# Kernel optimization log

Measured on AMD Instinct MI355X. Metric: run time of the kernel, lower is better.

The kernel has to match this reference:

```python
import jax, jax.numpy as jnp
import numpy as np


def setup_inputs() -> dict:
    key = jax.random.key(0)
    ks = jax.random.split(key, 8)
    N, E = 10000, 160000
    IN, OUT, TC = 512, 512, 256
    x = jax.random.normal(ks[0], (N, IN), dtype=jnp.float32)
    t_emb = jax.random.normal(ks[1], (TC,), dtype=jnp.float32)
    edge_index = jax.random.randint(ks[2], (2, E), 0, N, dtype=jnp.int64)
    # GCNConv weight (glorot-ish scale) and bias
    W = jax.random.normal(ks[3], (IN, OUT), dtype=jnp.float32) / np.sqrt(IN)
    b = jnp.zeros((OUT,), dtype=jnp.float32)
    # time_proj Linear(TC, OUT)
    Wt = jax.random.normal(ks[4], (TC, OUT), dtype=jnp.float32) / np.sqrt(TC)
    bt = jnp.zeros((OUT,), dtype=jnp.float32)
    return {"x": x, "t_emb": t_emb, "edge_index": edge_index,
            "W": W, "b": b, "Wt": Wt, "bt": bt}


def _gcn_conv(x, edge_index, W, b):
    # PyG GCNConv: add self-loops, symmetric normalization, xW, scatter-add, +bias
    N = x.shape[0]
    loops = jnp.arange(N, dtype=edge_index.dtype)
    src = jnp.concatenate([edge_index[0], loops])  # [E+N]
    dst = jnp.concatenate([edge_index[1], loops])
    deg = jax.ops.segment_sum(jnp.ones_like(dst, dtype=x.dtype), dst,
                              num_segments=N)  # in-degree incl. self-loop
    dinv = jnp.where(deg > 0, jax.lax.rsqrt(deg), 0.0)
    norm = dinv[src] * dinv[dst]  # [E+N]
    xw = x @ W  # [N, OUT] - transform before gather (fewer FLOPs on edges)
    msgs = norm[:, None] * xw[src]  # [E+N, OUT]
    out = jax.ops.segment_sum(msgs, dst, num_segments=N)
    return out + b


def reference(x, t_emb, edge_index, W, b, Wt, bt):
    h = _gcn_conv(x, edge_index, W, b)          # [N, OUT]
    time_emb = t_emb @ Wt + bt                   # [OUT] (1-D t_emb branch)
    return h + time_emb
```

## Files before the change

kernel.cpp:

```cpp
#include <hip/hip_runtime.h>

#define OUTC 512
#define INC 512
#define NTILE 4
#define TCOL 128
#define LDA 72
#define TPB 256
#define CAP 96

typedef __bf16 bf16x8 __attribute__((ext_vector_type(8)));
typedef float f32x4 __attribute__((ext_vector_type(4)));

static __device__ __forceinline__ unsigned short f2bf(float f) {
    unsigned u = __float_as_uint(f);
    unsigned r = u + 0x7fffu + ((u >> 16) & 1u);
    return (unsigned short)(r >> 16);
}
static __device__ __forceinline__ float bflo(unsigned r) { return __uint_as_float(r << 16); }
static __device__ __forceinline__ float bfhi(unsigned r) { return __uint_as_float(r & 0xffff0000u); }
static __device__ __forceinline__ void acc8s(float* a, uint4 v, float n) {
    a[0] += n * bflo(v.x); a[1] += n * bfhi(v.x);
    a[2] += n * bflo(v.y); a[3] += n * bfhi(v.y);
    a[4] += n * bflo(v.z); a[5] += n * bfhi(v.z);
    a[6] += n * bflo(v.w); a[7] += n * bfhi(v.w);
}

__global__ __launch_bounds__(256) void k_prep(const float* __restrict__ x,
                                              const float* __restrict__ W,
                                              const float* __restrict__ t_emb,
                                              const float* __restrict__ Wt,
                                              const float* __restrict__ bt,
                                              const float* __restrict__ b,
                                              int* __restrict__ counts,
                                              unsigned short* __restrict__ xb,
                                              unsigned short* __restrict__ wtb,
                                              float* __restrict__ temb,
                                              int ZB, int XBB,
                                              int M, int Mpad, int TC) {
    __shared__ float smem[32 * 33];
    int bid = blockIdx.x;
    if (bid < ZB) {
        int i = bid * 256 + threadIdx.x;
        if (i < M) counts[i] = 0;
    } else if (bid < ZB + XBB) {
        int idx = (bid - ZB) * 256 + threadIdx.x;
        int row = idx >> 6;
        int kg = (idx & 63) * 8;
        ushort4 h0 = make_ushort4(0, 0, 0, 0), h1 = make_ushort4(0, 0, 0, 0);
        if (row < M) {
            float4 v0 = *(const float4*)(x + (size_t)row * INC + kg);
            float4 v1 = *(const float4*)(x + (size_t)row * INC + kg + 4);
            h0 = make_ushort4(f2bf(v0.x), f2bf(v0.y), f2bf(v0.z), f2bf(v0.w));
            h1 = make_ushort4(f2bf(v1.x), f2bf(v1.y), f2bf(v1.z), f2bf(v1.w));
        }
        *(ushort4*)(xb + (size_t)row * INC + kg) = h0;
        *(ushort4*)(xb + (size_t)row * INC + kg + 4) = h1;
    } else if (bid < ZB + XBB + 256) {
        int b2 = bid - (ZB + XBB);
        int bk = (b2 & 15) * 32, bn = (b2 >> 4) * 32;
        int tx = threadIdx.x & 31, ty = threadIdx.x >> 5;
        for (int r = ty; r < 32; r += 8)
            smem[r * 33 + tx] = W[(size_t)(bk + r) * OUTC + bn + tx];
        __syncthreads();
        for (int r = ty; r < 32; r += 8)
            wtb[(size_t)(bn + r) * INC + bk + tx] = f2bf(smem[tx * 33 + r]);
    } else {
        int j = bid - (ZB + XBB + 256);
        int t = threadIdx.x;
        float p = 0.0f;
        for (int k = t; k < TC; k += 256) p += t_emb[k] * Wt[(size_t)k * OUTC + j];
        smem[t] = p;
        __syncthreads();
        for (int s = 128; s > 0; s >>= 1) {
            if (t < s) smem[t] += smem[t + s];
            __syncthreads();
        }
        if (t == 0) temb[j] = smem[0] + bt[j] + b[j];
    }
}

__global__ __launch_bounds__(256) void k_ag(const unsigned short* __restrict__ xb,
                                            const unsigned short* __restrict__ wtb,
                                            unsigned short* __restrict__ xwb,
                                            const int* __restrict__ src,
                                            const int* __restrict__ dst,
                                            int* __restrict__ counts,
                                            int* __restrict__ slots,
                                            int E, int Mpad) {
    __shared__ unsigned short la[128 * LDA];
    __shared__ unsigned short lb[64 * LDA];

    const int bid = blockIdx.x;
    const int tid = threadIdx.x;
    const int GB = (Mpad / 128) * 8;

    if (bid >= GB) {
        int e = (bid - GB) * 256 + tid;
        if (e < E) {
            int s = src[e];
            int d = dst[e];
            int pos = atomicAdd(&counts[d], 1);
            if (pos < CAP) slots[(size_t)d * CAP + pos] = s;
        }
        return;
    }

    const int n0 = (bid & 7) * 64;
    const int m0 = (bid >> 3) * 128;
    const int lane = tid & 63;
    const int wave = tid >> 6;
    const int wm = wave * 32;
    const int l15 = lane & 15;
    const int k8 = (lane >> 4) * 8;

    f32x4 acc[2][4];
#pragma unroll
    for (int t = 0; t < 2; ++t)
#pragma unroll
        for (int u = 0; u < 4; ++u)
            acc[t][u] = (f32x4){0.f, 0.f, 0.f, 0.f};

    for (int k0 = 0; k0 < INC; k0 += 64) {
#pragma unroll
        for (int i = 0; i < 4; ++i) {
            int f = i * 256 + tid;
            int row = f >> 3, c = f & 7;
            uint4 v = *(const uint4*)(xb + (size_t)(m0 + row) * INC + k0 + c * 8);
            *(uint4*)(&la[row * LDA + c * 8]) = v;
        }
#pragma unroll
        for (int i = 0; i < 2; ++i) {
            int f = i * 256 + tid;
            int row = f >> 3, c = f & 7;
            uint4 v = *(const uint4*)(wtb + (size_t)(n0 + row) * INC + k0 + c * 8);
            *(uint4*)(&lb[row * LDA + c * 8]) = v;
        }
        __syncthreads();

#pragma unroll
        for (int kc = 0; kc < 64; kc += 32) {
            bf16x8 af0 = *(const bf16x8*)(&la[(wm + l15) * LDA + kc + k8]);
            bf16x8 af1 = *(const bf16x8*)(&la[(wm + 16 + l15) * LDA + kc + k8]);
#pragma unroll
            for (int u = 0; u < 4; ++u) {
                bf16x8 bfr = *(const bf16x8*)(&lb[(u * 16 + l15) * LDA + kc + k8]);
                acc[0][u] = __builtin_amdgcn_mfma_f32_16x16x32_bf16(af0, bfr, acc[0][u], 0, 0, 0);
                acc[1][u] = __builtin_amdgcn_mfma_f32_16x16x32_bf16(af1, bfr, acc[1][u], 0, 0, 0);
            }
        }
        __syncthreads();
    }

    const int rbase = (lane >> 4) * 4;
#pragma unroll
    for (int t = 0; t < 2; ++t)
#pragma unroll
        for (int u = 0; u < 4; ++u) {
            int gcol = n0 + u * 16 + l15;
            unsigned short* p = xwb + (size_t)(gcol >> 7) * Mpad * TCOL + (gcol & 127);
#pragma unroll
            for (int r = 0; r < 4; ++r) {
                int grow = m0 + wm + t * 16 + rbase + r;
                p[(size_t)grow * TCOL] = f2bf(acc[t][u][r]);
            }
        }
}

__global__ __launch_bounds__(256) void k_gather(const int* __restrict__ slots,
                                                const int* __restrict__ counts,
                                                const unsigned short* __restrict__ xwb,
                                                const float* __restrict__ temb,
                                                float* __restrict__ out, int N, int Mpad) {
    const int bid = blockIdx.x;
    const int tile = (bid & 7) >> 1;
    const int node = (bid >> 3) * 8 + (bid & 1) * 4 + (threadIdx.x >> 6);
    if (node >= N) return;
    const int lane = threadIdx.x & 63;
    const int slot = lane >> 4;
    const int c8 = (lane & 15) * 8;
    const unsigned short* basep = xwb + (size_t)tile * Mpad * TCOL + c8;

    float a[8] = {0.f, 0.f, 0.f, 0.f, 0.f, 0.f, 0.f, 0.f};
    const int deg = counts[node];
    const int dc = deg < CAP ? deg : CAP;
    const int* sp = slots + (size_t)node * CAP;
    int i = 0;
    for (; i + 8 <= dc; i += 8) {
        int sA = sp[i + slot];
        int sB = sp[i + 4 + slot];
        uint4 vA = *(const uint4*)(basep + (size_t)sA * TCOL);
        uint4 vB = *(const uint4*)(basep + (size_t)sB * TCOL);
        float nA = rsqrtf((float)counts[sA] + 1.0f);
        float nB = rsqrtf((float)counts[sB] + 1.0f);
        acc8s(a, vA, nA);
        acc8s(a, vB, nB);
    }
    for (; i < dc; i += 4) {
        int idx = i + slot;
        int sA = node;
        float nA = 0.f;
        if (idx < dc) {
            sA = sp[idx];
            nA = rsqrtf((float)counts[sA] + 1.0f);
        }
        uint4 v = *(const uint4*)(basep + (size_t)sA * TCOL);
        acc8s(a, v, nA);
    }
#pragma unroll
    for (int k = 0; k < 8; ++k) {
        a[k] += __shfl_xor(a[k], 16, 64);
        a[k] += __shfl_xor(a[k], 32, 64);
    }
    const float di = rsqrtf((float)deg + 1.0f);
    {
        uint4 v = *(const uint4*)(basep + (size_t)node * TCOL);
        acc8s(a, v, di);
    }
    if (slot < 2) {
        const int gc = tile * TCOL + c8 + slot * 4;
        float4 tv = *(const float4*)(temb + gc);
        float4 o;
        o.x = di * a[slot * 4 + 0] + tv.x;
        o.y = di * a[slot * 4 + 1] + tv.y;
        o.z = di * a[slot * 4 + 2] + tv.z;
        o.w = di * a[slot * 4 + 3] + tv.w;
        *(float4*)(out + (size_t)node * OUTC + gc) = o;
    }
}

extern "C" void kernel_launch(void* const* d_in, const int* in_sizes, int n_in,
                              void* d_out, int out_size, void* d_ws, size_t ws_size,
                              hipStream_t stream) {
    const float* x     = (const float*)d_in[0];
    const float* t_emb = (const float*)d_in[1];
    const int*   ei    = (const int*)d_in[2];
    const float* W     = (const float*)d_in[3];
    const float* b     = (const float*)d_in[4];
    const float* Wt    = (const float*)d_in[5];
    const float* bt    = (const float*)d_in[6];
    float* out = (float*)d_out;

    const int N  = in_sizes[0] / INC;
    const int E  = in_sizes[2] / 2;
    const int TC = in_sizes[1];
    const int Mpad = (N + 127) & ~127;

    char* ws = (char*)d_ws;
    size_t off = 0;
    unsigned short* xb  = (unsigned short*)(ws + off); off += (size_t)Mpad * INC * 2;
    unsigned short* xwb = (unsigned short*)(ws + off); off += (size_t)Mpad * OUTC * 2;
    unsigned short* wtb = (unsigned short*)(ws + off); off += (size_t)INC * OUTC * 2;
    int* counts = (int*)(ws + off);        off += ((size_t)N * 4 + 255) & ~(size_t)255;
    int* slots  = (int*)(ws + off);        off += ((size_t)N * CAP * 4 + 255) & ~(size_t)255;
    float* temb = (float*)(ws + off);      off += OUTC * 4;

    const int* srcIdx = ei;
    const int* dstIdx = ei + E;

    const int ZB  = (N + 255) / 256;
    const int XBB = Mpad * (INC / 8) / 256;
    const int GB  = (Mpad / 128) * 8;
    const int SB  = (E + 255) / 256;

    k_prep<<<ZB + XBB + 256 + OUTC, TPB, 0, stream>>>(x, W, t_emb, Wt, bt, b,
                                                      counts, xb, wtb, temb,
                                                      ZB, XBB, N, Mpad, TC);
    k_ag<<<GB + SB, TPB, 0, stream>>>(xb, wtb, xwb, srcIdx, dstIdx,
                                      counts, slots, E, Mpad);

    const int gather_blocks = ((N + 7) / 8) * 8;
    k_gather<<<gather_blocks, TPB, 0, stream>>>(slots, counts, xwb,
                                                temb, out, N, Mpad);
}
```

Baseline: 133.6 us.

## Fuse fp32-to-bf16 conversion of x into GEMM tile load and remap block order

Removes the separate pass that converted x to a bf16 workspace copy. The GEMM kernel now reads fp32 x directly, converts it to bf16 while staging into LDS, and zero-pads rows past N. This drops one full write and re-read of a 10MB intermediate. In exchange each x element is read in fp32 (twice the bytes) by all 8 column-tile blocks, and conversion ALU moves into the GEMM loop. The block-to-tile mapping is also permuted so that consecutive blocks cover different row tiles, which changes L2 reuse of x across column tiles.

```diff
diff --git a/kernel.cpp b/kernel.cpp
--- a/kernel.cpp
+++ b/kernel.cpp
@@ -16,6 +16,9 @@
     unsigned r = u + 0x7fffu + ((u >> 16) & 1u);
     return (unsigned short)(r >> 16);
 }
+static __device__ __forceinline__ unsigned f2bf2(float lo, float hi) {
+    return (unsigned)f2bf(lo) | ((unsigned)f2bf(hi) << 16);
+}
 static __device__ __forceinline__ float bflo(unsigned r) { return __uint_as_float(r << 16); }
 static __device__ __forceinline__ float bfhi(unsigned r) { return __uint_as_float(r & 0xffff0000u); }
 static __device__ __forceinline__ void acc8s(float* a, uint4 v, float n) {
@@ -25,38 +28,22 @@
     a[6] += n * bflo(v.w); a[7] += n * bfhi(v.w);
 }
 
-__global__ __launch_bounds__(256) void k_prep(const float* __restrict__ x,
-                                              const float* __restrict__ W,
+__global__ __launch_bounds__(256) void k_prep(const float* __restrict__ W,
                                               const float* __restrict__ t_emb,
                                               const float* __restrict__ Wt,
                                               const float* __restrict__ bt,
                                               const float* __restrict__ b,
                                               int* __restrict__ counts,
-                                              unsigned short* __restrict__ xb,
                                               unsigned short* __restrict__ wtb,
                                               float* __restrict__ temb,
-                                              int ZB, int XBB,
-                                              int M, int Mpad, int TC) {
+                                              int ZB, int M, int TC) {
     __shared__ float smem[32 * 33];
     int bid = blockIdx.x;
     if (bid < ZB) {
         int i = bid * 256 + threadIdx.x;
         if (i < M) counts[i] = 0;
-    } else if (bid < ZB + XBB) {
-        int idx = (bid - ZB) * 256 + threadIdx.x;
-        int row = idx >> 6;
-        int kg = (idx & 63) * 8;
-        ushort4 h0 = make_ushort4(0, 0, 0, 0), h1 = make_ushort4(0, 0, 0, 0);
-        if (row < M) {
-            float4 v0 = *(const float4*)(x + (size_t)row * INC + kg);
-            float4 v1 = *(const float4*)(x + (size_t)row * INC + kg + 4);
-            h0 = make_ushort4(f2bf(v0.x), f2bf(v0.y), f2bf(v0.z), f2bf(v0.w));
-            h1 = make_ushort4(f2bf(v1.x), f2bf(v1.y), f2bf(v1.z), f2bf(v1.w));
-        }
-        *(ushort4*)(xb + (size_t)row * INC + kg) = h0;
-        *(ushort4*)(xb + (size_t)row * INC + kg + 4) = h1;
-    } else if (bid < ZB + XBB + 256) {
-        int b2 = bid - (ZB + XBB);
+    } else if (bid < ZB + 256) {
+        int b2 = bid - ZB;
         int bk = (b2 & 15) * 32, bn = (b2 >> 4) * 32;
         int tx = threadIdx.x & 31, ty = threadIdx.x >> 5;
         for (int r = ty; r < 32; r += 8)
@@ -65,7 +52,7 @@
         for (int r = ty; r < 32; r += 8)
             wtb[(size_t)(bn + r) * INC + bk + tx] = f2bf(smem[tx * 33 + r]);
     } else {
-        int j = bid - (ZB + XBB + 256);
+        int j = bid - (ZB + 256);
         int t = threadIdx.x;
         float p = 0.0f;
         for (int k = t; k < TC; k += 256) p += t_emb[k] * Wt[(size_t)k * OUTC + j];
@@ -79,20 +66,21 @@
     }
 }
 
-__global__ __launch_bounds__(256) void k_ag(const unsigned short* __restrict__ xb,
+__global__ __launch_bounds__(256) void k_ag(const float* __restrict__ x,
                                             const unsigned short* __restrict__ wtb,
                                             unsigned short* __restrict__ xwb,
                                             const int* __restrict__ src,
                                             const int* __restrict__ dst,
                                             int* __restrict__ counts,
                                             int* __restrict__ slots,
-                                            int E, int Mpad) {
+                                            int E, int N, int Mpad) {
     __shared__ unsigned short la[128 * LDA];
     __shared__ unsigned short lb[64 * LDA];
 
     const int bid = blockIdx.x;
     const int tid = threadIdx.x;
-    const int GB = (Mpad / 128) * 8;
+    const int MB = Mpad / 128;
+    const int GB = MB * 8;
 
     if (bid >= GB) {
         int e = (bid - GB) * 256 + tid;
@@ -105,8 +93,9 @@
         return;
     }
 
-    const int n0 = (bid & 7) * 64;
-    const int m0 = (bid >> 3) * 128;
+    const int T = (bid & 7) * MB + (bid >> 3);
+    const int m0 = (T >> 3) * 128;
+    const int n0 = (T & 7) * 64;
     const int lane = tid & 63;
     const int wave = tid >> 6;
     const int wm = wave * 32;
@@ -125,8 +114,18 @@
         for (int i = 0; i < 4; ++i) {
             int f = i * 256 + tid;
             int row = f >> 3, c = f & 7;
-            uint4 v = *(const uint4*)(xb + (size_t)(m0 + row) * INC + k0 + c * 8);
-            *(uint4*)(&la[row * LDA + c * 8]) = v;
+            int grow = m0 + row;
+            uint4 h = make_uint4(0, 0, 0, 0);
+            if (grow < N) {
+                const float* xp = x + (size_t)grow * INC + k0 + c * 8;
+                float4 v0 = *(const float4*)(xp);
+                float4 v1 = *(const float4*)(xp + 4);
+                h.x = f2bf2(v0.x, v0.y);
+                h.y = f2bf2(v0.z, v0.w);
+                h.z = f2bf2(v1.x, v1.y);
+                h.w = f2bf2(v1.z, v1.w);
+            }
+            *(uint4*)(&la[row * LDA + c * 8]) = h;
         }
 #pragma unroll
         for (int i = 0; i < 2; ++i) {
@@ -247,7 +246,6 @@
 
     char* ws = (char*)d_ws;
     size_t off = 0;
-    unsigned short* xb  = (unsigned short*)(ws + off); off += (size_t)Mpad * INC * 2;
     unsigned short* xwb = (unsigned short*)(ws + off); off += (size_t)Mpad * OUTC * 2;
     unsigned short* wtb = (unsigned short*)(ws + off); off += (size_t)INC * OUTC * 2;
     int* counts = (int*)(ws + off);        off += ((size_t)N * 4 + 255) & ~(size_t)255;
@@ -257,16 +255,14 @@
     const int* srcIdx = ei;
     const int* dstIdx = ei + E;
 
-    const int ZB  = (N + 255) / 256;
-    const int XBB = Mpad * (INC / 8) / 256;
-    const int GB  = (Mpad / 128) * 8;
-    const int SB  = (E + 255) / 256;
-
-    k_prep<<<ZB + XBB + 256 + OUTC, TPB, 0, stream>>>(x, W, t_emb, Wt, bt, b,
-                                                      counts, xb, wtb, temb,
-                                                      ZB, XBB, N, Mpad, TC);
-    k_ag<<<GB + SB, TPB, 0, stream>>>(xb, wtb, xwb, srcIdx, dstIdx,
-                                      counts, slots, E, Mpad);
+    const int ZB = (N + 255) / 256;
+    const int GB = (Mpad / 128) * 8;
+    const int SB = (E + 255) / 256;
+
+    k_prep<<<ZB + 256 + OUTC, TPB, 0, stream>>>(W, t_emb, Wt, bt, b,
+                                                counts, wtb, temb, ZB, N, TC);
+    k_ag<<<GB + SB, TPB, 0, stream>>>(x, wtb, xwb, srcIdx, dstIdx,
+                                      counts, slots, E, N, Mpad);
 
     const int gather_blocks = ((N + 7) / 8) * 8;
     k_gather<<<gather_blocks, TPB, 0, stream>>>(slots, counts, xwb,
```

Result: slower. 138.2 us (+3.4%).
